# Kernel optimization log

Hardware: AMD Instinct MI355X
Metric: run time of the kernel (lower is better)

The kernel has to match this reference:

```python
import jax, jax.numpy as jnp
import numpy as np

B, V, J, NB = 1024, 3889, 33, 10
P = (J - 1) * 9  # 288 pose-blendshape basis


def setup_inputs() -> dict:
    key = jax.random.key(0)
    ks = jax.random.split(key, 9)
    n = lambda k, s, sc=1.0: jax.random.normal(k, s, dtype=jnp.float32) * sc
    betas = n(ks[0], (B, NB))
    global_orient = n(ks[1], (B, 3), 0.5)
    body_pose = n(ks[2], (B, (J - 1) * 3), 0.3)
    transl = n(ks[3], (B, 3))
    v_template = n(ks[4], (V, 3))
    shapedirs = n(ks[5], (V, 3, NB), 0.01)
    posedirs = n(ks[6], (P, V * 3), 0.01)
    jr = jax.random.uniform(ks[7], (J, V), dtype=jnp.float32)
    J_regressor = jr / jnp.sum(jr, axis=1, keepdims=True)  # rows sum to 1
    w = jax.random.uniform(ks[8], (V, J), dtype=jnp.float32)
    lbs_weights = w / jnp.sum(w, axis=1, keepdims=True)
    # kinematic tree: chain, parents[i] < i; root parent handled specially
    parents = np.maximum(np.arange(J) - 1, 0).astype(np.int64)
    return {"betas": betas, "global_orient": global_orient, "body_pose": body_pose,
            "transl": transl, "v_template": v_template, "shapedirs": shapedirs,
            "posedirs": posedirs, "J_regressor": J_regressor,
            "lbs_weights": lbs_weights, "parents": parents}


def _rodrigues(rot_vecs):
    """Axis-angle [.., 3] -> rotation matrices [.., 3, 3] (Rodrigues)."""
    angle = jnp.linalg.norm(rot_vecs + 1e-8, axis=-1, keepdims=True)
    axis = rot_vecs / angle
    rx, ry, rz = axis[..., 0], axis[..., 1], axis[..., 2]
    z = jnp.zeros_like(rx)
    K = jnp.stack([z, -rz, ry, rz, z, -rx, -ry, rx, z], axis=-1)
    K = K.reshape(rot_vecs.shape[:-1] + (3, 3))
    s = jnp.sin(angle)[..., None]
    c = jnp.cos(angle)[..., None]
    return jnp.eye(3, dtype=rot_vecs.dtype) + s * K + (1.0 - c) * (K @ K)


def _lbs(betas, global_orient, body_pose, transl, v_template, shapedirs,
         posedirs, J_regressor, lbs_weights, parents):
    Bn = betas.shape[0]
    par = np.asarray(parents)  # static kinematic tree
    Jn = par.shape[0]
    # shape blendshapes
    v_shaped = v_template[None] + jnp.einsum('bl,vcl->bvc', betas, shapedirs)
    joints = jnp.einsum('jv,bvc->bjc', J_regressor, v_shaped)  # [B,J,3]
    # pose -> rotation matrices
    full_pose = jnp.concatenate([global_orient, body_pose], axis=1).reshape(Bn, Jn, 3)
    rot = _rodrigues(full_pose)  # [B,J,3,3]
    # pose blendshapes (identity-subtracted, root excluded)
    pose_feat = (rot[:, 1:] - jnp.eye(3, dtype=rot.dtype)).reshape(Bn, -1)  # [B,288]
    v_posed = v_shaped + (pose_feat @ posedirs).reshape(Bn, -1, 3)
    # forward kinematics: compose 4x4 transforms along the tree
    rel = joints.at[:, 1:].add(-joints[:, par[1:]])  # relative joint locations
    Tmat = jnp.concatenate([rot, rel[..., None]], axis=-1)  # [B,J,3,4]
    bottom = jnp.broadcast_to(jnp.array([0., 0., 0., 1.], Tmat.dtype), (Bn, Jn, 1, 4))
    Tmat = jnp.concatenate([Tmat, bottom], axis=2)  # [B,J,4,4]
    chain = [Tmat[:, 0]]
    for i in range(1, Jn):  # fixed small loop over joints
        chain.append(chain[int(par[i])] @ Tmat[:, i])
    transforms = jnp.stack(chain, axis=1)  # [B,J,4,4]
    # remove rest-pose joint locations from the transforms
    jh = jnp.concatenate([joints, jnp.zeros((Bn, Jn, 1), joints.dtype)], axis=-1)[..., None]
    A = transforms - jnp.pad(transforms @ jh, ((0, 0), (0, 0), (0, 0), (3, 0)))
    # linear blend skinning
    T = jnp.einsum('vj,bjmn->bvmn', lbs_weights, A)  # [B,V,4,4]
    vh = jnp.concatenate([v_posed, jnp.ones(v_posed.shape[:-1] + (1,), v_posed.dtype)], axis=-1)
    verts = jnp.einsum('bvmn,bvn->bvm', T, vh)[..., :3]
    return verts + transl[:, None]


def reference(betas, global_orient, body_pose, transl, v_template, shapedirs,
              posedirs, J_regressor, lbs_weights, parents):
    return _lbs(betas, global_orient, body_pose, transl, v_template, shapedirs,
                posedirs, J_regressor, lbs_weights, parents)
```

## Files before the change

### kernel.cpp

```cpp
#include <hip/hip_runtime.h>
#include <math.h>

#define B_  1024
#define V_  3889
#define J_  33
#define NB_ 10
#define P_  288
#define N3  11667
#define NT_ 122
#define NPAD (NT_*96)

typedef short bf16x8 __attribute__((ext_vector_type(8)));
typedef float f32x4  __attribute__((ext_vector_type(4)));

__device__ __forceinline__ unsigned short f2bf(float f) {
  union { float f; unsigned u; } v; v.f = f;
  unsigned r = v.u + 0x7FFFu + ((v.u >> 16) & 1u);
  return (unsigned short)(r >> 16);
}
__device__ __forceinline__ float bf2f(unsigned short h) {
  union { unsigned u; float f; } v; v.u = ((unsigned)h) << 16; return v.f;
}

#define PREP_JS   33
#define PREP_CVT  399
#define PREP_NB   463

__global__ __launch_bounds__(256) void k_prep(
    const float* __restrict__ Jreg, const float* __restrict__ vt,
    const float* __restrict__ sd, const float* __restrict__ pdirs,
    const float* __restrict__ lbsw,
    float* __restrict__ JS, float* __restrict__ bj,
    unsigned short* __restrict__ pdT, unsigned short* __restrict__ wbf)
{
  __shared__ __align__(16) unsigned char su[38016];
  const int bid = blockIdx.x;
  const int t = threadIdx.x;

  if (bid < PREP_JS) {
    float* red = (float*)su;
    const int j = bid;
    if (t < 128) {
      float acc[33];
      #pragma unroll
      for (int e = 0; e < 33; ++e) acc[e] = 0.f;
      for (int v = t; v < V_; v += 128) {
        float r = Jreg[j*V_ + v];
        #pragma unroll
        for (int c = 0; c < 3; ++c) {
          acc[c*11 + 10] += r * vt[v*3 + c];
          #pragma unroll
          for (int l = 0; l < NB_; ++l)
            acc[c*11 + l] += r * sd[v*30 + c*10 + l];
        }
      }
      #pragma unroll
      for (int e = 0; e < 33; ++e) red[e*128 + t] = acc[e];
    }
    __syncthreads();
    if (t < 33) {
      float s = 0.f;
      for (int i = 0; i < 128; ++i) s += red[t*128 + i];
      int c = t / 11, l = t % 11;
      if (l == 10) bj[j*3 + c] = s;
      else         JS[(j*3 + c)*NB_ + l] = s;
    }
  } else if (bid < PREP_CVT) {
    float* tile = (float*)su;
    const int bb = bid - PREP_JS;
    const int nt = bb / 3;
    const int c0 = (bb % 3) * 32;
    for (int i = t; i < P_*32; i += 256) {
      int k = i >> 5, c = i & 31;
      int gc = nt*96 + c0 + c;
      tile[k*33 + c] = (gc < N3) ? pdirs[(size_t)k*N3 + gc] : 0.f;
    }
    __syncthreads();
    for (int o = t; o < 32*P_; o += 256) {
      int c = o / P_, k = o % P_;
      pdT[((size_t)(nt*96 + c0 + c))*P_ + k] = f2bf(tile[k*33 + c]);
    }
  } else {
    const int bb = bid - PREP_CVT;
    const int total = 4096*96;
    for (int i = bb*256 + t; i < total; i += 64*256) {
      int v = i / 96, k = i - 96*v;
      float val = 0.f;
      if (v < V_) {
        if (k < 33) val = lbsw[(size_t)v*33 + k];
        else if (k < 66) {
          float w = lbsw[(size_t)v*33 + (k-33)];
          val = w - bf2f(f2bf(w));
        }
      }
      wbf[i] = f2bf(val);
    }
  }
}

__global__ __launch_bounds__(64) void k_pose(
    const float* __restrict__ betas, const float* __restrict__ go,
    const float* __restrict__ bp, const float* __restrict__ JS,
    const float* __restrict__ bj,
    unsigned short* __restrict__ pfb,
    unsigned short* __restrict__ Abf)
{
  const int b = blockIdx.x;
  const int t = threadIdx.x;
  __shared__ float rot[J_][9];
  __shared__ float jnt[J_][3];
  __shared__ float Ash[J_][12];
  __shared__ float bsh[NB_];
  if (t < NB_) bsh[t] = betas[b*NB_ + t];
  __syncthreads();
  if (t < J_) {
    #pragma unroll
    for (int c = 0; c < 3; ++c) {
      float s = bj[t*3 + c];
      #pragma unroll
      for (int l = 0; l < NB_; ++l) s += bsh[l] * JS[(t*3 + c)*NB_ + l];
      jnt[t][c] = s;
    }
    float px, py, pz;
    if (t == 0) { px = go[b*3+0]; py = go[b*3+1]; pz = go[b*3+2]; }
    else {
      const float* p = bp + (size_t)b*((J_-1)*3) + (t-1)*3;
      px = p[0]; py = p[1]; pz = p[2];
    }
    float ax = px + 1e-8f, ay = py + 1e-8f, az = pz + 1e-8f;
    float ang = sqrtf(ax*ax + ay*ay + az*az);
    float inv = 1.0f / ang;
    float ux = px*inv, uy = py*inv, uz = pz*inv;
    float sn = sinf(ang), cs = cosf(ang);
    float K[9] = {0.f,-uz,uy,  uz,0.f,-ux,  -uy,ux,0.f};
    float R[9];
    #pragma unroll
    for (int r = 0; r < 3; ++r)
      #pragma unroll
      for (int c = 0; c < 3; ++c) {
        float k2 = K[r*3+0]*K[0*3+c] + K[r*3+1]*K[1*3+c] + K[r*3+2]*K[2*3+c];
        float id = (r == c) ? 1.f : 0.f;
        R[r*3+c] = id + sn*K[r*3+c] + (1.f - cs)*k2;
      }
    #pragma unroll
    for (int e = 0; e < 9; ++e) rot[t][e] = R[e];
    if (t >= 1) {
      #pragma unroll
      for (int e = 0; e < 9; ++e)
        pfb[(size_t)b*P_ + (t-1)*9 + e] = f2bf(R[e] - ((e==0||e==4||e==8) ? 1.f : 0.f));
    }
  }
  __syncthreads();
  if (t == 0) {
    float G[12];
    #pragma unroll
    for (int r = 0; r < 3; ++r) {
      G[r*4+0] = rot[0][r*3+0]; G[r*4+1] = rot[0][r*3+1];
      G[r*4+2] = rot[0][r*3+2]; G[r*4+3] = jnt[0][r];
    }
    for (int j = 0; j < J_; ++j) {
      if (j > 0) {
        float rel0 = jnt[j][0] - jnt[j-1][0];
        float rel1 = jnt[j][1] - jnt[j-1][1];
        float rel2 = jnt[j][2] - jnt[j-1][2];
        float N[12];
        #pragma unroll
        for (int r = 0; r < 3; ++r) {
          #pragma unroll
          for (int c = 0; c < 3; ++c)
            N[r*4+c] = G[r*4+0]*rot[j][0*3+c] + G[r*4+1]*rot[j][1*3+c] + G[r*4+2]*rot[j][2*3+c];
          N[r*4+3] = G[r*4+0]*rel0 + G[r*4+1]*rel1 + G[r*4+2]*rel2 + G[r*4+3];
        }
        #pragma unroll
        for (int e = 0; e < 12; ++e) G[e] = N[e];
      }
      #pragma unroll
      for (int r = 0; r < 3; ++r) {
        Ash[j][r*4+0] = G[r*4+0];
        Ash[j][r*4+1] = G[r*4+1];
        Ash[j][r*4+2] = G[r*4+2];
        Ash[j][r*4+3] = G[r*4+3] - (G[r*4+0]*jnt[j][0] + G[r*4+1]*jnt[j][1] + G[r*4+2]*jnt[j][2]);
      }
    }
  }
  __syncthreads();
  const float* Af = &Ash[0][0];
  for (int i = t; i < 1536; i += 64) {
    int n = i / 96, k = i - 96*n;
    int j = (k < 33) ? k : ((k < 66) ? (k - 33) : -1);
    float val = 0.f;
    if (j >= 0) {
      if (n < 12) val = Af[j*12 + n];
      else if (n < 15) {
        float tr = Af[j*12 + (n-12)*4 + 3];
        val = tr - bf2f(f2bf(tr));
      }
    }
    Abf[(size_t)b*1536 + i] = f2bf(val);
  }
}

#define TS 17

__global__ __launch_bounds__(256, 2) void k_gs(
    const float* __restrict__ betas,
    const float* __restrict__ vt, const float* __restrict__ sd,
    const unsigned short* __restrict__ pdT,
    const unsigned short* __restrict__ pfb_g,
    const float* __restrict__ transl,
    const unsigned short* __restrict__ wbf,
    const unsigned short* __restrict__ Abf,
    float* __restrict__ out)
{
  __shared__ float s_beta[640];
  __shared__ float s_vp[64*100];
  __shared__ float s_T[4][2*32*TS];

  const int tid = threadIdx.x;
  const int nt = blockIdx.x, bt = blockIdx.y;
  const int b0 = bt*64;
  const int lane = tid & 63, wid = tid >> 6;
  const int wm = wid >> 1, wn = wid & 1;
  const int l15 = lane & 15, lg = lane >> 4;

  for (int i = tid; i < 64*NB_; i += 256) s_beta[i] = betas[(size_t)b0*NB_ + i];
  __syncthreads();

  f32x4 acc[2][3];
  #pragma unroll
  for (int f = 0; f < 3; ++f) {
    int colL = wn*48 + f*16 + l15;
    int gc = nt*96 + colL;
    if (gc < N3) {
      int v = gc/3, c = gc - 3*v;
      float base = vt[gc];
      float sval[2][4];
      #pragma unroll
      for (int mi = 0; mi < 2; ++mi)
        #pragma unroll
        for (int reg = 0; reg < 4; ++reg) sval[mi][reg] = base;
      #pragma unroll
      for (int l = 0; l < NB_; ++l) {
        float sdv = sd[(size_t)v*30 + c*10 + l];
        #pragma unroll
        for (int mi = 0; mi < 2; ++mi) {
          int row_b = mi*32 + wm*16 + lg*4;
          #pragma unroll
          for (int reg = 0; reg < 4; ++reg)
            sval[mi][reg] += s_beta[(row_b+reg)*NB_ + l] * sdv;
        }
      }
      #pragma unroll
      for (int mi = 0; mi < 2; ++mi) {
        acc[mi][f][0]=sval[mi][0]; acc[mi][f][1]=sval[mi][1];
        acc[mi][f][2]=sval[mi][2]; acc[mi][f][3]=sval[mi][3];
      }
    } else {
      #pragma unroll
      for (int mi = 0; mi < 2; ++mi)
        acc[mi][f] = (f32x4){0.f,0.f,0.f,0.f};
    }
  }

  const unsigned short* __restrict__ pfrow0 =
      pfb_g + (size_t)(b0 + wm*16 + l15)*P_ + lg*8;
  const unsigned short* __restrict__ pfrow1 =
      pfb_g + (size_t)(b0 + 32 + wm*16 + l15)*P_ + lg*8;
  const unsigned short* __restrict__ pdrow =
      pdT + (size_t)(nt*96 + wn*48 + l15)*P_ + lg*8;
  #pragma unroll
  for (int ks = 0; ks < 9; ++ks) {
    bf16x8 a0 = *(const bf16x8*)(pfrow0 + ks*32);
    bf16x8 a1 = *(const bf16x8*)(pfrow1 + ks*32);
    #pragma unroll
    for (int f = 0; f < 3; ++f) {
      bf16x8 b = *(const bf16x8*)(pdrow + (size_t)f*16*P_ + ks*32);
      acc[0][f] = __builtin_amdgcn_mfma_f32_16x16x32_bf16(a0, b, acc[0][f], 0, 0, 0);
      acc[1][f] = __builtin_amdgcn_mfma_f32_16x16x32_bf16(a1, b, acc[1][f], 0, 0, 0);
    }
  }

  #pragma unroll
  for (int f = 0; f < 3; ++f) {
    int colL = wn*48 + f*16 + l15;
    #pragma unroll
    for (int mi = 0; mi < 2; ++mi) {
      int row_b = mi*32 + wm*16 + lg*4;
      #pragma unroll
      for (int reg = 0; reg < 4; ++reg)
        s_vp[(row_b+reg)*100 + colL] = acc[mi][f][reg];
    }
  }
  __syncthreads();

  bf16x8 afr[2][3];
  #pragma unroll
  for (int mt = 0; mt < 2; ++mt) {
    const int vrow = nt*32 + mt*16 + l15;
    #pragma unroll
    for (int ks = 0; ks < 3; ++ks)
      afr[mt][ks] = *(const bf16x8*)&wbf[(size_t)vrow*96 + ks*32 + lg*8];
  }

  float* Tw = &s_T[wid][0];
  const int h2 = lane >> 5, vl = lane & 31;
  const int v = nt*32 + vl;

  for (int g = 0; g < 8; ++g) {
    #pragma unroll
    for (int h = 0; h < 2; ++h) {
      const int b = b0 + wid*16 + g*2 + h;
      const unsigned short* Ab = Abf + (size_t)b*1536;
      bf16x8 bfr[3];
      #pragma unroll
      for (int ks = 0; ks < 3; ++ks)
        bfr[ks] = *(const bf16x8*)&Ab[l15*96 + ks*32 + lg*8];
      f32x4 t0 = {0.f,0.f,0.f,0.f}, t1 = t0;
      #pragma unroll
      for (int ks = 0; ks < 3; ++ks) {
        t0 = __builtin_amdgcn_mfma_f32_16x16x32_bf16(afr[0][ks], bfr[ks], t0, 0, 0, 0);
        t1 = __builtin_amdgcn_mfma_f32_16x16x32_bf16(afr[1][ks], bfr[ks], t1, 0, 0, 0);
      }
      #pragma unroll
      for (int reg = 0; reg < 4; ++reg) {
        Tw[h*32*TS + (lg*4+reg)*TS + l15]      = t0[reg];
        Tw[h*32*TS + (16+lg*4+reg)*TS + l15]   = t1[reg];
      }
    }
    {
      const int bl2 = wid*16 + g*2 + h2;
      const int b2  = b0 + bl2;
      const float* Tr = Tw + h2*32*TS + vl*TS;
      float px = s_vp[bl2*100 + vl*3 + 0];
      float py = s_vp[bl2*100 + vl*3 + 1];
      float pz = s_vp[bl2*100 + vl*3 + 2];
      float o0 = Tr[0]*px + Tr[1]*py + Tr[2]*pz  + Tr[3]  + Tr[12] + transl[b2*3+0];
      float o1 = Tr[4]*px + Tr[5]*py + Tr[6]*pz  + Tr[7]  + Tr[13] + transl[b2*3+1];
      float o2 = Tr[8]*px + Tr[9]*py + Tr[10]*pz + Tr[11] + Tr[14] + transl[b2*3+2];
      if (v < V_) {
        size_t po = (size_t)b2*N3 + (size_t)v*3;
        out[po+0] = o0; out[po+1] = o1; out[po+2] = o2;
      }
    }
  }
}

extern "C" void kernel_launch(void* const* d_in, const int* in_sizes, int n_in,
                              void* d_out, int out_size, void* d_ws, size_t ws_size,
                              hipStream_t stream) {
  const float* betas  = (const float*)d_in[0];
  const float* go     = (const float*)d_in[1];
  const float* bp     = (const float*)d_in[2];
  const float* transl = (const float*)d_in[3];
  const float* vt     = (const float*)d_in[4];
  const float* sd     = (const float*)d_in[5];
  const float* pdirs  = (const float*)d_in[6];
  const float* Jreg   = (const float*)d_in[7];
  const float* lbsw   = (const float*)d_in[8];
  float* out = (float*)d_out;
  char* wb = (char*)d_ws;

  float* JS            = (float*)(wb + 0);
  float* bj            = (float*)(wb + 4096);
  unsigned short* pfb  = (unsigned short*)(wb + 1630720);
  unsigned short* Abf  = (unsigned short*)(wb + 2221056);
  unsigned short* pdT  = (unsigned short*)(wb + 5366784);
  unsigned short* wbf  = (unsigned short*)(wb + 12112896);

  hipLaunchKernelGGL(k_prep, dim3(PREP_NB), dim3(256), 0, stream,
                     Jreg, vt, sd, pdirs, lbsw, JS, bj, pdT, wbf);
  hipLaunchKernelGGL(k_pose, dim3(B_), dim3(64), 0, stream,
                     betas, go, bp, JS, bj, pfb, Abf);
  hipLaunchKernelGGL(k_gs,   dim3(NT_, B_/64), dim3(256), 0, stream,
                     betas, vt, sd, pdT, pfb, transl, wbf, Abf, out);
}
```

Baseline: 110.5 us.

## Software-pipeline A-matrix and posed-vertex loads in skinning loop

Moves the skinning-weight fragment load ahead of the first barrier. Prefetches the next batch pair's bf16 transform fragments and posed-vertex values while the current pair is computed, and stages transl in shared memory. The goal is to hide global load latency behind MFMA work in the per-batch skinning loop. The cost is extra registers for the double buffers, which could lower occupancy under launch_bounds(256,2).

New measurement: 105.5 us. -4.6%, faster.

```diff
diff --git a/kernel.cpp b/kernel.cpp
--- a/kernel.cpp
+++ b/kernel.cpp
@@ -213,6 +213,7 @@
     float* __restrict__ out)
 {
   __shared__ float s_beta[640];
+  __shared__ float s_tr[192];
   __shared__ float s_vp[64*100];
   __shared__ float s_T[4][2*32*TS];
 
@@ -224,6 +225,16 @@
   const int l15 = lane & 15, lg = lane >> 4;
 
   for (int i = tid; i < 64*NB_; i += 256) s_beta[i] = betas[(size_t)b0*NB_ + i];
+  for (int i = tid; i < 192; i += 256) s_tr[i] = transl[(size_t)b0*3 + i];
+
+  bf16x8 afr[2][3];
+  #pragma unroll
+  for (int mt = 0; mt < 2; ++mt) {
+    const int vrow = nt*32 + mt*16 + l15;
+    #pragma unroll
+    for (int ks = 0; ks < 3; ++ks)
+      afr[mt][ks] = *(const bf16x8*)&wbf[(size_t)vrow*96 + ks*32 + lg*8];
+  }
   __syncthreads();
 
   f32x4 acc[2][3];
@@ -280,6 +291,15 @@
     }
   }
 
+  bf16x8 bcur[2][3];
+  #pragma unroll
+  for (int h = 0; h < 2; ++h) {
+    const unsigned short* Ab = Abf + (size_t)(b0 + wid*16 + h)*1536;
+    #pragma unroll
+    for (int ks = 0; ks < 3; ++ks)
+      bcur[h][ks] = *(const bf16x8*)&Ab[l15*96 + ks*32 + lg*8];
+  }
+
   #pragma unroll
   for (int f = 0; f < 3; ++f) {
     int colL = wn*48 + f*16 + l15;
@@ -293,33 +313,39 @@
   }
   __syncthreads();
 
-  bf16x8 afr[2][3];
-  #pragma unroll
-  for (int mt = 0; mt < 2; ++mt) {
-    const int vrow = nt*32 + mt*16 + l15;
-    #pragma unroll
-    for (int ks = 0; ks < 3; ++ks)
-      afr[mt][ks] = *(const bf16x8*)&wbf[(size_t)vrow*96 + ks*32 + lg*8];
-  }
-
   float* Tw = &s_T[wid][0];
   const int h2 = lane >> 5, vl = lane & 31;
   const int v = nt*32 + vl;
 
+  float pxc = s_vp[(wid*16 + h2)*100 + vl*3 + 0];
+  float pyc = s_vp[(wid*16 + h2)*100 + vl*3 + 1];
+  float pzc = s_vp[(wid*16 + h2)*100 + vl*3 + 2];
+
+  #pragma unroll 2
   for (int g = 0; g < 8; ++g) {
+    bf16x8 bnxt[2][3];
+    float pxn = 0.f, pyn = 0.f, pzn = 0.f;
+    if (g < 7) {
+      #pragma unroll
+      for (int h = 0; h < 2; ++h) {
+        const unsigned short* Ab = Abf + (size_t)(b0 + wid*16 + (g+1)*2 + h)*1536;
+        #pragma unroll
+        for (int ks = 0; ks < 3; ++ks)
+          bnxt[h][ks] = *(const bf16x8*)&Ab[l15*96 + ks*32 + lg*8];
+      }
+      int bln = wid*16 + (g+1)*2 + h2;
+      pxn = s_vp[bln*100 + vl*3 + 0];
+      pyn = s_vp[bln*100 + vl*3 + 1];
+      pzn = s_vp[bln*100 + vl*3 + 2];
+    }
+
     #pragma unroll
     for (int h = 0; h < 2; ++h) {
-      const int b = b0 + wid*16 + g*2 + h;
-      const unsigned short* Ab = Abf + (size_t)b*1536;
-      bf16x8 bfr[3];
-      #pragma unroll
-      for (int ks = 0; ks < 3; ++ks)
-        bfr[ks] = *(const bf16x8*)&Ab[l15*96 + ks*32 + lg*8];
       f32x4 t0 = {0.f,0.f,0.f,0.f}, t1 = t0;
       #pragma unroll
       for (int ks = 0; ks < 3; ++ks) {
-        t0 = __builtin_amdgcn_mfma_f32_16x16x32_bf16(afr[0][ks], bfr[ks], t0, 0, 0, 0);
-        t1 = __builtin_amdgcn_mfma_f32_16x16x32_bf16(afr[1][ks], bfr[ks], t1, 0, 0, 0);
+        t0 = __builtin_amdgcn_mfma_f32_16x16x32_bf16(afr[0][ks], bcur[h][ks], t0, 0, 0, 0);
+        t1 = __builtin_amdgcn_mfma_f32_16x16x32_bf16(afr[1][ks], bcur[h][ks], t1, 0, 0, 0);
       }
       #pragma unroll
       for (int reg = 0; reg < 4; ++reg) {
@@ -331,16 +357,21 @@
       const int bl2 = wid*16 + g*2 + h2;
       const int b2  = b0 + bl2;
       const float* Tr = Tw + h2*32*TS + vl*TS;
-      float px = s_vp[bl2*100 + vl*3 + 0];
-      float py = s_vp[bl2*100 + vl*3 + 1];
-      float pz = s_vp[bl2*100 + vl*3 + 2];
-      float o0 = Tr[0]*px + Tr[1]*py + Tr[2]*pz  + Tr[3]  + Tr[12] + transl[b2*3+0];
-      float o1 = Tr[4]*px + Tr[5]*py + Tr[6]*pz  + Tr[7]  + Tr[13] + transl[b2*3+1];
-      float o2 = Tr[8]*px + Tr[9]*py + Tr[10]*pz + Tr[11] + Tr[14] + transl[b2*3+2];
+      float o0 = Tr[0]*pxc + Tr[1]*pyc + Tr[2]*pzc  + Tr[3]  + Tr[12] + s_tr[bl2*3+0];
+      float o1 = Tr[4]*pxc + Tr[5]*pyc + Tr[6]*pzc  + Tr[7]  + Tr[13] + s_tr[bl2*3+1];
+      float o2 = Tr[8]*pxc + Tr[9]*pyc + Tr[10]*pzc + Tr[11] + Tr[14] + s_tr[bl2*3+2];
       if (v < V_) {
         size_t po = (size_t)b2*N3 + (size_t)v*3;
         out[po+0] = o0; out[po+1] = o1; out[po+2] = o2;
       }
+    }
+    if (g < 7) {
+      #pragma unroll
+      for (int h = 0; h < 2; ++h)
+        #pragma unroll
+        for (int ks = 0; ks < 3; ++ks)
+          bcur[h][ks] = bnxt[h][ks];
+      pxc = pxn; pyc = pyn; pzc = pzn;
     }
   }
 }
```
